# Kernel tuning notes

Measured on AMD Instinct MI355X. Metric: run time of the kernel, lower is better.

Reference implementation:

```python
import jax, jax.numpy as jnp
import numpy as np

DIM = 768
NUM_HEADS = 12
HEAD_DIM = DIM // NUM_HEADS
H, W = 16, 64
HK, WK = 7, 11
N = H * W
B = 8
SCALE = HEAD_DIM ** -0.5


def build_local_mask():
    # Vectorized version of the original nested loop: for each token (h,w),
    # positions inside the hk x wk window are visible (0), others -inf.
    h_idx = np.repeat(np.arange(H), W)  # [N]
    w_idx = np.tile(np.arange(W), H)    # [N]
    hh = np.arange(H + HK - 1)
    ww = np.arange(W + WK - 1)
    in_h = (hh[None, :] >= h_idx[:, None]) & (hh[None, :] < h_idx[:, None] + HK)  # [N, H+hk-1]
    in_w = (ww[None, :] >= w_idx[:, None]) & (ww[None, :] < w_idx[:, None] + WK)  # [N, W+wk-1]
    visible = in_h[:, :, None] & in_w[:, None, :]  # [N, H+hk-1, W+wk-1]
    mask_big = np.where(visible, 0.0, 1.0).astype(np.float32)
    mask_crop = mask_big[:, HK // 2:H + HK // 2, WK // 2:W + WK // 2].reshape(N, N)
    mask = np.where(mask_crop < 1.0, mask_crop, np.float32(-np.inf))  # [N, N]
    return jnp.asarray(mask)[None, None]  # [1, 1, N, N]


def setup_inputs() -> dict:
    key = jax.random.key(0)
    k1, k2, k3 = jax.random.split(key, 3)
    x = jax.random.normal(k1, (B, N, DIM), dtype=jnp.float32)
    w_qkv = jax.random.normal(k2, (3 * DIM, DIM), dtype=jnp.float32) * 0.02  # torch Linear weight [out,in]
    w_proj = jax.random.normal(k3, (DIM, DIM), dtype=jnp.float32) * 0.02
    b_proj = jnp.zeros((DIM,), dtype=jnp.float32)
    mask = build_local_mask()
    return {"x": x, "w_qkv": w_qkv, "w_proj": w_proj, "b_proj": b_proj, "mask": mask}


def reference(x, w_qkv, w_proj, b_proj, mask):
    Bx, Nx, C = x.shape
    qkv = jnp.einsum('bnc,oc->bno', x, w_qkv)  # [B, N, 3*dim]
    qkv = qkv.reshape(Bx, Nx, 3, NUM_HEADS, HEAD_DIM).transpose(2, 0, 3, 1, 4)  # [3,B,h,N,d]
    q, k, v = qkv[0] * SCALE, qkv[1], qkv[2]
    attn = jnp.einsum('bhnd,bhmd->bhnm', q, k) + mask  # [B,h,N,N] with local -inf mask
    attn = jax.nn.softmax(attn, axis=-1)
    out = jnp.einsum('bhnm,bhmd->bhnd', attn, v)  # [B,h,N,d]
    out = out.transpose(0, 2, 1, 3).reshape(Bx, Nx, C)
    out = jnp.einsum('bnc,oc->bno', out, w_proj) + b_proj
    return out
```

## Files before the change

### kernel.cpp

```cpp
#include <hip/hip_runtime.h>
#include <hip/hip_bf16.h>
#include <stdint.h>

typedef __bf16 bf16;
typedef __bf16 bf16x8 __attribute__((ext_vector_type(8)));
typedef __bf16 bf16x4 __attribute__((ext_vector_type(4)));
typedef float f32x4 __attribute__((ext_vector_type(4)));

#define KDIM 768
#define NHEAD 12
#define HDIM 64
#define NTOK 1024
#define BATCH 8

#define SWZ(row, b) ((b) ^ (((row) & 7) << 4))

__device__ __forceinline__ void gl_lds16(const bf16* g, bf16* l) {
    __builtin_amdgcn_global_load_lds((const __attribute__((address_space(1))) void*)g,
                                     (__attribute__((address_space(3))) void*)l, 16, 0, 0);
}

#define G_MFMA(a, b, c) __builtin_amdgcn_mfma_f32_16x16x32_bf16(a, b, c, 0, 0, 0)
#define VMW(N) asm volatile("s_waitcnt vmcnt(" #N ")" ::: "memory")

__global__ void k_cvt_all(const float* __restrict__ x, const float* __restrict__ wq,
                          const float* __restrict__ wp, bf16* __restrict__ xb,
                          bf16* __restrict__ wqb, bf16* __restrict__ wpb) {
    int b = blockIdx.x;
    const float* src;
    bf16* dst;
    int base;
    if (b < 6144)       { src = x;  dst = xb;  base = b; }
    else if (b < 7872)  { src = wq; dst = wqb; base = b - 6144; }
    else                { src = wp; dst = wpb; base = b - 7872; }
    int i = (base * 256 + threadIdx.x) * 4;
    float4 v = *(const float4*)(src + i);
    bf16x4 o;
    o[0] = (bf16)v.x; o[1] = (bf16)v.y; o[2] = (bf16)v.z; o[3] = (bf16)v.w;
    *(bf16x4*)(dst + i) = o;
}


#define QTILE(S, kA, kB, doA, doB, vmn) do {                                    \
    const char* A8 = (const char*)sA[S];                                        \
    const char* B8 = (const char*)sB[S];                                        \
    bf16x8 af[2], bfr[6];                                                       \
    af[0] = *(const bf16x8*)(A8 + (wr * 64 + 0 + lr) * 64 + kxoff);             \
    af[1] = *(const bf16x8*)(A8 + (wr * 64 + 16 + lr) * 64 + kxoff);            \
    _Pragma("unroll")                                                           \
    for (int n = 0; n < 6; ++n)                                                 \
        bfr[n] = *(const bf16x8*)(B8 + (wc * 96 + n * 16 + lr) * 64 + kxoff);   \
    if (doA) {                                                                  \
        const bf16* p_ = Ast + (size_t)(kA) * 32;                               \
        gl_lds16(p_,                    &sA[(S) ^ 1][t * 8]);                   \
        gl_lds16(p_ + (size_t)64 * KDIM, &sA[(S) ^ 1][t * 8 + 2048]);           \
    }                                                                           \
    __builtin_amdgcn_s_setprio(1);                                              \
    _Pragma("unroll")                                                           \
    for (int m = 0; m < 2; ++m)                                                 \
        _Pragma("unroll")                                                       \
        for (int n = 0; n < 6; ++n)                                             \
            acc[m][n] = G_MFMA(af[m], bfr[n], acc[m][n]);                       \
    __builtin_amdgcn_s_setprio(0);                                              \
    __builtin_amdgcn_s_barrier();                                               \
    af[0] = *(const bf16x8*)(A8 + (wr * 64 + 32 + lr) * 64 + kxoff);            \
    af[1] = *(const bf16x8*)(A8 + (wr * 64 + 48 + lr) * 64 + kxoff);            \
    if (doB) {                                                                  \
        const bf16* p_ = Wst + (size_t)(kB) * 32;                               \
        gl_lds16(p_,                     &sB[S][t * 8]);                        \
        gl_lds16(p_ + (size_t)64 * KDIM,  &sB[S][t * 8 + 2048]);                \
        gl_lds16(p_ + (size_t)128 * KDIM, &sB[S][t * 8 + 4096]);                \
    }                                                                           \
    __builtin_amdgcn_s_setprio(1);                                              \
    _Pragma("unroll")                                                           \
    for (int m = 0; m < 2; ++m)                                                 \
        _Pragma("unroll")                                                       \
        for (int n = 0; n < 6; ++n)                                             \
            acc[m + 2][n] = G_MFMA(af[m], bfr[n], acc[m + 2][n]);               \
    __builtin_amdgcn_s_setprio(0);                                              \
    if ((vmn) == 3) { VMW(3); } else if ((vmn) == 0) { VMW(0); }                \
    __builtin_amdgcn_s_barrier();                                               \
} while (0)

__global__ __launch_bounds__(256, 3) void k_gemm_qkv(
    const bf16* __restrict__ A, const bf16* __restrict__ W,
    bf16* __restrict__ qb, bf16* __restrict__ kb, bf16* __restrict__ vb)
{
    __shared__ __attribute__((aligned(16))) bf16 sA[2][4096];
    __shared__ __attribute__((aligned(16))) bf16 sB[2][6144];
    const int t = threadIdx.x;
    const int lane = t & 63;
    const int wv = t >> 6;
    const int wr = wv >> 1, wc = wv & 1;
    const int lr = lane & 15, lg = lane >> 4;
    const int kxoff = (lg << 4) ^ (((lr >> 1) & 3) << 4);
    const int srow = t >> 2;
    const int spos = ((t & 3) ^ ((t >> 3) & 3)) * 8;
    const int bm = blockIdx.x, bn = blockIdx.y;
    const bf16* Ab = A + (size_t)bm * 128 * KDIM;
    const bf16* Wb = W + (size_t)bn * 192 * KDIM;
    const bf16* Ast = Ab + (size_t)srow * KDIM + spos;
    const bf16* Wst = Wb + (size_t)srow * KDIM + spos;
    f32x4 acc[4][6] = {};

    gl_lds16(Ast,                     &sA[0][t * 8]);
    gl_lds16(Ast + (size_t)64 * KDIM, &sA[0][t * 8 + 2048]);
    gl_lds16(Wst,                      &sB[0][t * 8]);
    gl_lds16(Wst + (size_t)64 * KDIM,  &sB[0][t * 8 + 2048]);
    gl_lds16(Wst + (size_t)128 * KDIM, &sB[0][t * 8 + 4096]);
    gl_lds16(Wst + 32,                      &sB[1][t * 8]);
    gl_lds16(Wst + 32 + (size_t)64 * KDIM,  &sB[1][t * 8 + 2048]);
    gl_lds16(Wst + 32 + (size_t)128 * KDIM, &sB[1][t * 8 + 4096]);
    VMW(3);
    __builtin_amdgcn_s_barrier();

#pragma unroll 1
    for (int g = 0; g < 11; ++g) {
        QTILE(0, 2 * g + 1, 2 * g + 2, 1, 1, 3);
        QTILE(1, 2 * g + 2, 2 * g + 3, 1, 1, 3);
    }
    QTILE(0, 23, 0, 1, 0, 0);
    QTILE(1, 0, 0, 0, 0, -1);

    const float QSC = 0.18033688011112042f;
#pragma unroll
    for (int n = 0; n < 6; ++n) {
        int o = bn * 192 + wc * 96 + n * 16 + lr;
        int s = o / 768;
        int rem = o - s * 768;
        int head = rem >> 6;
        int d = o & 63;
        bf16* dst = (s == 0) ? qb : ((s == 1) ? kb : vb);
        float sc = (s == 0) ? QSC : 1.0f;
#pragma unroll
        for (int m = 0; m < 4; ++m) {
            int grow = bm * 128 + wr * 64 + m * 16 + lg * 4;
            int bidx = grow >> 10;
            int tok = grow & 1023;
            size_t base = (((size_t)bidx * NHEAD + head) * NTOK + tok) * HDIM + d;
#pragma unroll
            for (int r = 0; r < 4; ++r)
                dst[base + (size_t)r * HDIM] = (bf16)(acc[m][n][r] * sc);
        }
    }
}

#define P_STAGE(Ab, Wb, Abuf, Bbuf, k0) do {                                    \
    gl_lds16((Ab) + (size_t)sr0 * KDIM + (k0) + sc0, (Abuf) + wv * 512);        \
    gl_lds16((Ab) + (size_t)sr1 * KDIM + (k0) + sc1, (Abuf) + 2048 + wv * 512); \
    gl_lds16((Wb) + (size_t)sr0 * KDIM + (k0) + sc0, (Bbuf) + wv * 512);        \
    gl_lds16((Wb) + (size_t)sr1 * KDIM + (k0) + sc1, (Bbuf) + 2048 + wv * 512); \
} while (0)

__global__ __launch_bounds__(256) void k_gemm_proj(
    const bf16* __restrict__ A, const bf16* __restrict__ W,
    const float* __restrict__ bias, float* __restrict__ out)
{
    __shared__ bf16 As[2][4096];
    __shared__ bf16 Bs[2][4096];
    const int t = threadIdx.x;
    const int lane = t & 63;
    const int wv = t >> 6;
    const int wr = wv >> 1, wc = wv & 1;
    const int lr = lane & 15, lg = lane >> 4;
    const int q0 = wv * 64 + lane;
    const int R0 = q0 >> 3, wp0 = (q0 & 7) ^ (R0 & 7);
    const int sr0 = 2 * R0 + (wp0 >> 2), sc0 = (wp0 & 3) * 8;
    const int q1 = 256 + wv * 64 + lane;
    const int R1 = q1 >> 3, wp1 = (q1 & 7) ^ (R1 & 7);
    const int sr1 = 2 * R1 + (wp1 >> 2), sc1 = (wp1 & 3) * 8;
    const int rhalf = lr >> 1;
    const int xorp = (((lr & 1) * 64 + lg * 16) ^ (rhalf << 4));
    const int bm = blockIdx.x, bn = blockIdx.y;
    const bf16* Ab = A + (size_t)bm * 128 * KDIM;
    const bf16* Wb = W + (size_t)bn * 128 * KDIM;

    f32x4 acc[4][4] = {};
    P_STAGE(Ab, Wb, As[0], Bs[0], 0);
    P_STAGE(Ab, Wb, As[1], Bs[1], 32);
    VMW(4);
    __builtin_amdgcn_s_barrier();
#pragma unroll 1
    for (int tt = 0; tt < 24; ++tt) {
        int p = tt & 1;
        const char* Ab8 = (const char*)As[p];
        const char* Bb8 = (const char*)Bs[p];
        bf16x8 af[4], bfr[4];
#pragma unroll
        for (int m = 0; m < 4; ++m)
            af[m] = *(const bf16x8*)(Ab8 + (wr * 32 + m * 8 + rhalf) * 128 + xorp);
#pragma unroll
        for (int n = 0; n < 4; ++n)
            bfr[n] = *(const bf16x8*)(Bb8 + (wc * 32 + n * 8 + rhalf) * 128 + xorp);
        asm volatile("s_waitcnt lgkmcnt(0)" ::: "memory");
        __builtin_amdgcn_s_barrier();
        if (tt < 22) {
            P_STAGE(Ab, Wb, As[p], Bs[p], (tt + 2) * 32);
            __builtin_amdgcn_sched_barrier(0);
        }
#pragma unroll
        for (int m = 0; m < 4; ++m)
#pragma unroll
            for (int n = 0; n < 4; ++n)
                acc[m][n] = G_MFMA(af[m], bfr[n], acc[m][n]);
        if (tt < 22)       { VMW(4); }
        else if (tt == 22) { VMW(0); }
        __builtin_amdgcn_s_barrier();
    }

#pragma unroll
    for (int n = 0; n < 4; ++n) {
        int col = bn * 128 + wc * 64 + n * 16 + lr;
        float bv = bias[col];
#pragma unroll
        for (int m = 0; m < 4; ++m) {
            int grow = bm * 128 + wr * 64 + m * 16 + lg * 4;
#pragma unroll
            for (int r = 0; r < 4; ++r)
                out[(size_t)(grow + r) * KDIM + col] = acc[m][n][r] + bv;
        }
    }
}

__global__ __launch_bounds__(256) void k_attn(
    const bf16* __restrict__ qbuf, const bf16* __restrict__ kbuf,
    const bf16* __restrict__ vbuf, bf16* __restrict__ ob)
{
    const int x = blockIdx.x;
    const int sub = x >> 3;
    const int bh = (x & 7) * 12 + (sub >> 4);
    const int qblk = sub & 15;
    const int head = bh % NHEAD, bidx = bh / NHEAD;
    const bf16* Q  = qbuf + (size_t)bh * NTOK * HDIM;
    const bf16* Kp = kbuf + (size_t)bh * NTOK * HDIM;
    const bf16* Vp = vbuf + (size_t)bh * NTOK * HDIM;

    const int t = threadIdx.x, lane = t & 63, wv = t >> 6;
    const int lr = lane & 15, lg = lane >> 4, lkb = lg * 8;

    __shared__ bf16 Ks[2][64 * 64];
    __shared__ bf16 vT[2][64 * 64];
    __shared__ bf16 pls[4][16 * 64];

    {
        bf16x8 z = {};
        *(bf16x8*)&pls[wv][lane * 16] = z;
        *(bf16x8*)&pls[wv][lane * 16 + 8] = z;
    }

    bf16x8 qf[2];
#pragma unroll
    for (int ks = 0; ks < 2; ++ks)
        qf[ks] = *(const bf16x8*)(Q + (size_t)(qblk * 64 + wv * 16 + lr) * HDIM + ks * 32 + lkb);

    f32x4 acc[4] = {};
    float mrow[4] = {-1e30f, -1e30f, -1e30f, -1e30f};
    float lrow[4] = {0.f, 0.f, 0.f, 0.f};

    const int kh0 = (qblk - 3 < 0) ? 0 : qblk - 3;
    const int kh1 = (qblk + 3 > 15) ? 15 : qblk + 3;

    const int sj = t >> 2;
    const int sd = (t & 3) * 16;

    const bf16* ks0 = Kp + (size_t)(kh0 * 64 + sj) * HDIM + sd;
    const bf16* vs0 = Vp + (size_t)(kh0 * 64 + sj) * HDIM + sd;
    bf16x8 gk0 = *(const bf16x8*)ks0, gk1 = *(const bf16x8*)(ks0 + 8);
    bf16x8 gv0 = *(const bf16x8*)vs0, gv1 = *(const bf16x8*)(vs0 + 8);

    char* pb8 = (char*)pls[wv];
    const int wq0 = wv * 16 + lg * 4;
    int cur = 0;

    for (int kh = kh0; kh <= kh1; ++kh) {
        char* kb8 = (char*)Ks[cur];
        char* vb8 = (char*)vT[cur];
        {
            int kbo = sj * 128 + sd * 2;
            *(bf16x8*)(kb8 + SWZ(sj, kbo)) = gk0;
            *(bf16x8*)(kb8 + SWZ(sj, kbo + 16)) = gk1;
        }
#pragma unroll
        for (int ii = 0; ii < 8; ++ii) {
            int d = sd + ii;
            *(bf16*)(vb8 + SWZ(d, (d << 7) + (sj << 1))) = gv0[ii];
        }
#pragma unroll
        for (int ii = 0; ii < 8; ++ii) {
            int d = sd + 8 + ii;
            *(bf16*)(vb8 + SWZ(d, (d << 7) + (sj << 1))) = gv1[ii];
        }
        if (kh < kh1) {
            const bf16* kn = Kp + (size_t)((kh + 1) * 64 + sj) * HDIM + sd;
            const bf16* vn = Vp + (size_t)((kh + 1) * 64 + sj) * HDIM + sd;
            gk0 = *(const bf16x8*)kn; gk1 = *(const bf16x8*)(kn + 8);
            gv0 = *(const bf16x8*)vn; gv1 = *(const bf16x8*)(vn + 8);
        }
        asm volatile("s_waitcnt lgkmcnt(0)" ::: "memory");
        __builtin_amdgcn_s_barrier();

        f32x4 s[3];
#pragma unroll
        for (int jj = 0; jj < 3; ++jj) {
            int j = wv - 1 + jj;
            if (j >= 0 && j <= 3) {
                int key = j * 16 + lr;
                int kbase = key * 128;
                bf16x8 kf0 = *(const bf16x8*)(kb8 + SWZ(key, kbase + lg * 16));
                bf16x8 kf1 = *(const bf16x8*)(kb8 + SWZ(key, kbase + 64 + lg * 16));
                f32x4 sv = {};
                sv = __builtin_amdgcn_mfma_f32_16x16x32_bf16(qf[0], kf0, sv, 0, 0, 0);
                sv = __builtin_amdgcn_mfma_f32_16x16x32_bf16(qf[1], kf1, sv, 0, 0, 0);
#pragma unroll
                for (int r = 0; r < 4; ++r) {
                    int dw = wq0 + r - key;
                    sv[r] = (dw >= -5 && dw <= 5) ? sv[r] : -1e30f;
                }
                s[jj] = sv;
            } else {
                s[jj] = f32x4{-1e30f, -1e30f, -1e30f, -1e30f};
            }
        }

        float pm[4], scl[4];
#pragma unroll
        for (int r = 0; r < 4; ++r) pm[r] = fmaxf(fmaxf(s[0][r], s[1][r]), s[2][r]);
#pragma unroll
        for (int off = 1; off < 16; off <<= 1)
#pragma unroll
            for (int r = 0; r < 4; ++r) pm[r] = fmaxf(pm[r], __shfl_xor(pm[r], off));
#pragma unroll
        for (int r = 0; r < 4; ++r) {
            float mn = fmaxf(mrow[r], pm[r]);
            scl[r] = exp2f(mrow[r] - mn);
            mrow[r] = mn;
        }
#pragma unroll
        for (int dt = 0; dt < 4; ++dt)
#pragma unroll
            for (int r = 0; r < 4; ++r) acc[dt][r] *= scl[r];

        float psum[4] = {0.f, 0.f, 0.f, 0.f};
#pragma unroll
        for (int jj = 0; jj < 3; ++jj) {
            int j = wv - 1 + jj;
            if (j >= 0 && j <= 3) {
#pragma unroll
                for (int r = 0; r < 4; ++r) {
                    float p = exp2f(s[jj][r] - mrow[r]);
                    psum[r] += p;
                    int row = lg * 4 + r;
                    *(bf16*)(pb8 + SWZ(row, row * 128 + (j * 16 + lr) * 2)) = (bf16)p;
                }
            }
        }
#pragma unroll
        for (int r = 0; r < 4; ++r) lrow[r] = lrow[r] * scl[r] + psum[r];

        bf16x8 pf0 = *(const bf16x8*)(pb8 + SWZ(lr, lr * 128 + lg * 16));
        bf16x8 pf1 = *(const bf16x8*)(pb8 + SWZ(lr, lr * 128 + 64 + lg * 16));
#pragma unroll
        for (int dt = 0; dt < 4; ++dt) {
            int vrow = dt * 16 + lr;
            bf16x8 vf0 = *(const bf16x8*)(vb8 + SWZ(vrow, vrow * 128 + lg * 16));
            bf16x8 vf1 = *(const bf16x8*)(vb8 + SWZ(vrow, vrow * 128 + 64 + lg * 16));
            acc[dt] = __builtin_amdgcn_mfma_f32_16x16x32_bf16(pf0, vf0, acc[dt], 0, 0, 0);
            acc[dt] = __builtin_amdgcn_mfma_f32_16x16x32_bf16(pf1, vf1, acc[dt], 0, 0, 0);
        }
        cur ^= 1;
    }

#pragma unroll
    for (int off = 1; off < 16; off <<= 1)
#pragma unroll
        for (int r = 0; r < 4; ++r) lrow[r] += __shfl_xor(lrow[r], off);

#pragma unroll
    for (int r = 0; r < 4; ++r) {
        float inv = 1.0f / lrow[r];
        int tok = qblk * 64 + wv * 16 + lg * 4 + r;
        size_t rowbase = ((size_t)bidx * NTOK + tok) * KDIM + head * HDIM;
#pragma unroll
        for (int dt = 0; dt < 4; ++dt)
            ob[rowbase + dt * 16 + lr] = (bf16)(acc[dt][r] * inv);
    }
}

extern "C" void kernel_launch(void* const* d_in, const int* in_sizes, int n_in,
                              void* d_out, int out_size, void* d_ws, size_t ws_size,
                              hipStream_t stream) {
    const float* x      = (const float*)d_in[0];
    const float* w_qkv  = (const float*)d_in[1];
    const float* w_proj = (const float*)d_in[2];
    const float* b_proj = (const float*)d_in[3];
    float* out = (float*)d_out;

    char* ws = (char*)d_ws;
    bf16* xb  = (bf16*)(ws);
    bf16* wqb = (bf16*)(ws + 12582912);
    bf16* wpb = (bf16*)(ws + 16121856);
    bf16* qb  = (bf16*)(ws + 17301504);
    bf16* kb  = (bf16*)(ws + 29884416);
    bf16* vb  = (bf16*)(ws + 42467328);
    bf16* aob = (bf16*)(ws + 55050240);

    hipLaunchKernelGGL(k_cvt_all, dim3(8448), dim3(256), 0, stream, x, w_qkv, w_proj, xb, wqb, wpb);
    hipLaunchKernelGGL(k_gemm_qkv, dim3(64, 12), dim3(256), 0, stream, xb, wqb, qb, kb, vb);
    hipLaunchKernelGGL(k_attn,     dim3(1536), dim3(256), 0, stream, qb, kb, vb, aob);
    hipLaunchKernelGGL(k_gemm_proj, dim3(64, 6), dim3(256), 0, stream, aob, wpb, b_proj, out);
}
```

Baseline: 103.8 us.

## Fuse fp32 activation conversion into QKV GEMM and store interleaved QKV

The separate fp32-to-bf16 conversion of x is removed. The QKV GEMM now loads fp32 x into registers, converts it, and writes it to a triple-buffered LDS A tile, while the weights keep their async global-to-LDS path with a reworked wait schedule. The QKV output is written as a single token-major [B*N, 2304] buffer instead of head-split Q/K/V arrays, and attention reads from it with a 2304-element stride. This saves one full pass over x (read fp32, write and reread bf16), but it raises register pressure (occupancy hint drops from 3 to 2) and makes the attention K/V loads more strided.

```diff
diff --git a/kernel.cpp b/kernel.cpp
--- a/kernel.cpp
+++ b/kernel.cpp
@@ -12,6 +12,7 @@
 #define HDIM 64
 #define NTOK 1024
 #define BATCH 8
+#define QKVW 2304
 
 #define SWZ(row, b) ((b) ^ (((row) & 7) << 4))
 
@@ -23,16 +24,14 @@
 #define G_MFMA(a, b, c) __builtin_amdgcn_mfma_f32_16x16x32_bf16(a, b, c, 0, 0, 0)
 #define VMW(N) asm volatile("s_waitcnt vmcnt(" #N ")" ::: "memory")
 
-__global__ void k_cvt_all(const float* __restrict__ x, const float* __restrict__ wq,
-                          const float* __restrict__ wp, bf16* __restrict__ xb,
-                          bf16* __restrict__ wqb, bf16* __restrict__ wpb) {
+__global__ void k_cvt_w(const float* __restrict__ wq, const float* __restrict__ wp,
+                        bf16* __restrict__ wqb, bf16* __restrict__ wpb) {
     int b = blockIdx.x;
     const float* src;
     bf16* dst;
     int base;
-    if (b < 6144)       { src = x;  dst = xb;  base = b; }
-    else if (b < 7872)  { src = wq; dst = wqb; base = b - 6144; }
-    else                { src = wp; dst = wpb; base = b - 7872; }
+    if (b < 1728) { src = wq; dst = wqb; base = b; }
+    else          { src = wp; dst = wpb; base = b - 1728; }
     int i = (base * 256 + threadIdx.x) * 4;
     float4 v = *(const float4*)(src + i);
     bf16x4 o;
@@ -41,52 +40,74 @@
 }
 
 
-#define QTILE(S, kA, kB, doA, doB, vmn) do {                                    \
-    const char* A8 = (const char*)sA[S];                                        \
-    const char* B8 = (const char*)sB[S];                                        \
-    bf16x8 af[2], bfr[6];                                                       \
-    af[0] = *(const bf16x8*)(A8 + (wr * 64 + 0 + lr) * 64 + kxoff);             \
-    af[1] = *(const bf16x8*)(A8 + (wr * 64 + 16 + lr) * 64 + kxoff);            \
+#define AISS(R, kt) do {                                                        \
+    const float* p_ = Xst + (size_t)(kt) * 32;                                  \
+    R[0] = *(const float4*)(p_);                                                \
+    R[1] = *(const float4*)(p_ + 4);                                            \
+    R[2] = *(const float4*)(p_ + (size_t)64 * KDIM);                            \
+    R[3] = *(const float4*)(p_ + (size_t)64 * KDIM + 4);                        \
+} while (0)
+
+#define BISS(slot, kt) do {                                                     \
+    const bf16* p_ = Wst + (size_t)(kt) * 32;                                   \
+    gl_lds16(p_,                       &sB[slot][t * 8]);                       \
+    gl_lds16(p_ + (size_t)64 * KDIM,   &sB[slot][t * 8 + 2048]);                \
+    gl_lds16(p_ + (size_t)128 * KDIM,  &sB[slot][t * 8 + 4096]);                \
+} while (0)
+
+#define AWRT(R, slot) do {                                                      \
+    bf16x8 v0, v1;                                                              \
+    v0[0] = (bf16)R[0].x; v0[1] = (bf16)R[0].y; v0[2] = (bf16)R[0].z; v0[3] = (bf16)R[0].w; \
+    v0[4] = (bf16)R[1].x; v0[5] = (bf16)R[1].y; v0[6] = (bf16)R[1].z; v0[7] = (bf16)R[1].w; \
+    v1[0] = (bf16)R[2].x; v1[1] = (bf16)R[2].y; v1[2] = (bf16)R[2].z; v1[3] = (bf16)R[2].w; \
+    v1[4] = (bf16)R[3].x; v1[5] = (bf16)R[3].y; v1[6] = (bf16)R[3].z; v1[7] = (bf16)R[3].w; \
+    char* dp_ = (char*)&sA[0][0] + (slot) * 8192 + srow * 64 + swb;             \
+    *(bf16x8*)dp_ = v0;                                                         \
+    *(bf16x8*)(dp_ + 4096) = v1;                                                \
+} while (0)
+
+#define QTILE(ASL, BSL, RISS, RWRT, I_) do {                                    \
+    const int kt = g6 + (I_);                                                   \
+    const char* A8 = (const char*)sA[ASL];                                      \
+    const char* B8 = (const char*)sB[BSL];                                      \
+    bf16x8 af0 = *(const bf16x8*)(A8 + (wr * 64 +  0 + lr) * 64 + kxoff);       \
+    bf16x8 af1 = *(const bf16x8*)(A8 + (wr * 64 + 16 + lr) * 64 + kxoff);       \
+    bf16x8 af2 = *(const bf16x8*)(A8 + (wr * 64 + 32 + lr) * 64 + kxoff);       \
+    bf16x8 af3 = *(const bf16x8*)(A8 + (wr * 64 + 48 + lr) * 64 + kxoff);       \
+    bf16x8 bfr[6];                                                              \
     _Pragma("unroll")                                                           \
     for (int n = 0; n < 6; ++n)                                                 \
         bfr[n] = *(const bf16x8*)(B8 + (wc * 96 + n * 16 + lr) * 64 + kxoff);   \
-    if (doA) {                                                                  \
-        const bf16* p_ = Ast + (size_t)(kA) * 32;                               \
-        gl_lds16(p_,                    &sA[(S) ^ 1][t * 8]);                   \
-        gl_lds16(p_ + (size_t)64 * KDIM, &sA[(S) ^ 1][t * 8 + 2048]);           \
-    }                                                                           \
+    if (kt + 1 < 24) BISS((BSL) ^ 1, kt + 1);                                   \
+    if (kt + 2 < 24) AISS(RISS, kt + 2);                                        \
     __builtin_amdgcn_s_setprio(1);                                              \
     _Pragma("unroll")                                                           \
-    for (int m = 0; m < 2; ++m)                                                 \
-        _Pragma("unroll")                                                       \
-        for (int n = 0; n < 6; ++n)                                             \
-            acc[m][n] = G_MFMA(af[m], bfr[n], acc[m][n]);                       \
+    for (int n = 0; n < 6; ++n) {                                               \
+        acc[0][n] = G_MFMA(af0, bfr[n], acc[0][n]);                             \
+        acc[1][n] = G_MFMA(af1, bfr[n], acc[1][n]);                             \
+    }                                                                           \
     __builtin_amdgcn_s_setprio(0);                                              \
-    __builtin_amdgcn_s_barrier();                                               \
-    af[0] = *(const bf16x8*)(A8 + (wr * 64 + 32 + lr) * 64 + kxoff);            \
-    af[1] = *(const bf16x8*)(A8 + (wr * 64 + 48 + lr) * 64 + kxoff);            \
-    if (doB) {                                                                  \
-        const bf16* p_ = Wst + (size_t)(kB) * 32;                               \
-        gl_lds16(p_,                     &sB[S][t * 8]);                        \
-        gl_lds16(p_ + (size_t)64 * KDIM,  &sB[S][t * 8 + 2048]);                \
-        gl_lds16(p_ + (size_t)128 * KDIM, &sB[S][t * 8 + 4096]);                \
-    }                                                                           \
     __builtin_amdgcn_s_setprio(1);                                              \
     _Pragma("unroll")                                                           \
-    for (int m = 0; m < 2; ++m)                                                 \
-        _Pragma("unroll")                                                       \
-        for (int n = 0; n < 6; ++n)                                             \
-            acc[m + 2][n] = G_MFMA(af[m], bfr[n], acc[m + 2][n]);               \
+    for (int n = 0; n < 6; ++n) {                                               \
+        acc[2][n] = G_MFMA(af2, bfr[n], acc[2][n]);                             \
+        acc[3][n] = G_MFMA(af3, bfr[n], acc[3][n]);                             \
+    }                                                                           \
     __builtin_amdgcn_s_setprio(0);                                              \
-    if ((vmn) == 3) { VMW(3); } else if ((vmn) == 0) { VMW(0); }                \
-    __builtin_amdgcn_s_barrier();                                               \
+    if (kt < 22)       { VMW(4); }                                              \
+    else if (kt == 22) { VMW(0); }                                              \
+    if (kt < 23) {                                                              \
+        AWRT(RWRT, ((ASL) + 1) % 3);                                            \
+        asm volatile("s_waitcnt lgkmcnt(0)" ::: "memory");                      \
+        __builtin_amdgcn_s_barrier();                                           \
+    }                                                                           \
 } while (0)
 
-__global__ __launch_bounds__(256, 3) void k_gemm_qkv(
-    const bf16* __restrict__ A, const bf16* __restrict__ W,
-    bf16* __restrict__ qb, bf16* __restrict__ kb, bf16* __restrict__ vb)
+__global__ __launch_bounds__(256, 2) void k_gemm_qkv(
+    const float* __restrict__ X, const bf16* __restrict__ W,
+    bf16* __restrict__ qkvb)
 {
-    __shared__ __attribute__((aligned(16))) bf16 sA[2][4096];
+    __shared__ __attribute__((aligned(16))) bf16 sA[3][4096];
     __shared__ __attribute__((aligned(16))) bf16 sB[2][6144];
     const int t = threadIdx.x;
     const int lane = t & 63;
@@ -95,52 +116,45 @@
     const int lr = lane & 15, lg = lane >> 4;
     const int kxoff = (lg << 4) ^ (((lr >> 1) & 3) << 4);
     const int srow = t >> 2;
-    const int spos = ((t & 3) ^ ((t >> 3) & 3)) * 8;
+    const int swb = (((t & 3) ^ ((t >> 3) & 3))) << 4;
+    const int spos = (((t & 3) ^ ((t >> 3) & 3))) * 8;
     const int bm = blockIdx.x, bn = blockIdx.y;
-    const bf16* Ab = A + (size_t)bm * 128 * KDIM;
-    const bf16* Wb = W + (size_t)bn * 192 * KDIM;
-    const bf16* Ast = Ab + (size_t)srow * KDIM + spos;
-    const bf16* Wst = Wb + (size_t)srow * KDIM + spos;
+    const float* Xst = X + (size_t)(bm * 128 + srow) * KDIM + (t & 3) * 8;
+    const bf16* Wst  = W + (size_t)(bn * 192 + srow) * KDIM + spos;
     f32x4 acc[4][6] = {};
-
-    gl_lds16(Ast,                     &sA[0][t * 8]);
-    gl_lds16(Ast + (size_t)64 * KDIM, &sA[0][t * 8 + 2048]);
-    gl_lds16(Wst,                      &sB[0][t * 8]);
-    gl_lds16(Wst + (size_t)64 * KDIM,  &sB[0][t * 8 + 2048]);
-    gl_lds16(Wst + (size_t)128 * KDIM, &sB[0][t * 8 + 4096]);
-    gl_lds16(Wst + 32,                      &sB[1][t * 8]);
-    gl_lds16(Wst + 32 + (size_t)64 * KDIM,  &sB[1][t * 8 + 2048]);
-    gl_lds16(Wst + 32 + (size_t)128 * KDIM, &sB[1][t * 8 + 4096]);
+    float4 rE[4], rO[4];
+
+    AISS(rE, 0);
+    BISS(0, 0);
     VMW(3);
+    AWRT(rE, 0);
+    AISS(rE, 1);
+    VMW(4);
+    asm volatile("s_waitcnt lgkmcnt(0)" ::: "memory");
     __builtin_amdgcn_s_barrier();
 
 #pragma unroll 1
-    for (int g = 0; g < 11; ++g) {
-        QTILE(0, 2 * g + 1, 2 * g + 2, 1, 1, 3);
-        QTILE(1, 2 * g + 2, 2 * g + 3, 1, 1, 3);
-    }
-    QTILE(0, 23, 0, 1, 0, 0);
-    QTILE(1, 0, 0, 0, 0, -1);
+    for (int g = 0; g < 4; ++g) {
+        const int g6 = g * 6;
+        QTILE(0, 0, rO, rE, 0);
+        QTILE(1, 1, rE, rO, 1);
+        QTILE(2, 0, rO, rE, 2);
+        QTILE(0, 1, rE, rO, 3);
+        QTILE(1, 0, rO, rE, 4);
+        QTILE(2, 1, rE, rO, 5);
+    }
 
     const float QSC = 0.18033688011112042f;
 #pragma unroll
     for (int n = 0; n < 6; ++n) {
         int o = bn * 192 + wc * 96 + n * 16 + lr;
-        int s = o / 768;
-        int rem = o - s * 768;
-        int head = rem >> 6;
-        int d = o & 63;
-        bf16* dst = (s == 0) ? qb : ((s == 1) ? kb : vb);
-        float sc = (s == 0) ? QSC : 1.0f;
+        float sc = (o < 768) ? QSC : 1.0f;
 #pragma unroll
         for (int m = 0; m < 4; ++m) {
-            int grow = bm * 128 + wr * 64 + m * 16 + lg * 4;
-            int bidx = grow >> 10;
-            int tok = grow & 1023;
-            size_t base = (((size_t)bidx * NHEAD + head) * NTOK + tok) * HDIM + d;
+            int row = bm * 128 + wr * 64 + m * 16 + lg * 4;
 #pragma unroll
             for (int r = 0; r < 4; ++r)
-                dst[base + (size_t)r * HDIM] = (bf16)(acc[m][n][r] * sc);
+                qkvb[(size_t)(row + r) * QKVW + o] = (bf16)(acc[m][n][r] * sc);
         }
     }
 }
@@ -223,17 +237,14 @@
 }
 
 __global__ __launch_bounds__(256) void k_attn(
-    const bf16* __restrict__ qbuf, const bf16* __restrict__ kbuf,
-    const bf16* __restrict__ vbuf, bf16* __restrict__ ob)
+    const bf16* __restrict__ qkvb, bf16* __restrict__ ob)
 {
     const int x = blockIdx.x;
     const int sub = x >> 3;
     const int bh = (x & 7) * 12 + (sub >> 4);
     const int qblk = sub & 15;
     const int head = bh % NHEAD, bidx = bh / NHEAD;
-    const bf16* Q  = qbuf + (size_t)bh * NTOK * HDIM;
-    const bf16* Kp = kbuf + (size_t)bh * NTOK * HDIM;
-    const bf16* Vp = vbuf + (size_t)bh * NTOK * HDIM;
+    const bf16* BH = qkvb + (size_t)bidx * NTOK * QKVW + head * 64;
 
     const int t = threadIdx.x, lane = t & 63, wv = t >> 6;
     const int lr = lane & 15, lg = lane >> 4, lkb = lg * 8;
@@ -251,7 +262,7 @@
     bf16x8 qf[2];
 #pragma unroll
     for (int ks = 0; ks < 2; ++ks)
-        qf[ks] = *(const bf16x8*)(Q + (size_t)(qblk * 64 + wv * 16 + lr) * HDIM + ks * 32 + lkb);
+        qf[ks] = *(const bf16x8*)(BH + (size_t)(qblk * 64 + wv * 16 + lr) * QKVW + ks * 32 + lkb);
 
     f32x4 acc[4] = {};
     float mrow[4] = {-1e30f, -1e30f, -1e30f, -1e30f};
@@ -263,8 +274,8 @@
     const int sj = t >> 2;
     const int sd = (t & 3) * 16;
 
-    const bf16* ks0 = Kp + (size_t)(kh0 * 64 + sj) * HDIM + sd;
-    const bf16* vs0 = Vp + (size_t)(kh0 * 64 + sj) * HDIM + sd;
+    const bf16* ks0 = BH + 768 + (size_t)(kh0 * 64 + sj) * QKVW + sd;
+    const bf16* vs0 = BH + 1536 + (size_t)(kh0 * 64 + sj) * QKVW + sd;
     bf16x8 gk0 = *(const bf16x8*)ks0, gk1 = *(const bf16x8*)(ks0 + 8);
     bf16x8 gv0 = *(const bf16x8*)vs0, gv1 = *(const bf16x8*)(vs0 + 8);
 
@@ -291,8 +302,8 @@
             *(bf16*)(vb8 + SWZ(d, (d << 7) + (sj << 1))) = gv1[ii];
         }
         if (kh < kh1) {
-            const bf16* kn = Kp + (size_t)((kh + 1) * 64 + sj) * HDIM + sd;
-            const bf16* vn = Vp + (size_t)((kh + 1) * 64 + sj) * HDIM + sd;
+            const bf16* kn = BH + 768 + (size_t)((kh + 1) * 64 + sj) * QKVW + sd;
+            const bf16* vn = BH + 1536 + (size_t)((kh + 1) * 64 + sj) * QKVW + sd;
             gk0 = *(const bf16x8*)kn; gk1 = *(const bf16x8*)(kn + 8);
             gv0 = *(const bf16x8*)vn; gv1 = *(const bf16x8*)(vn + 8);
         }
@@ -396,16 +407,13 @@
     float* out = (float*)d_out;
 
     char* ws = (char*)d_ws;
-    bf16* xb  = (bf16*)(ws);
-    bf16* wqb = (bf16*)(ws + 12582912);
-    bf16* wpb = (bf16*)(ws + 16121856);
-    bf16* qb  = (bf16*)(ws + 17301504);
-    bf16* kb  = (bf16*)(ws + 29884416);
-    bf16* vb  = (bf16*)(ws + 42467328);
-    bf16* aob = (bf16*)(ws + 55050240);
-
-    hipLaunchKernelGGL(k_cvt_all, dim3(8448), dim3(256), 0, stream, x, w_qkv, w_proj, xb, wqb, wpb);
-    hipLaunchKernelGGL(k_gemm_qkv, dim3(64, 12), dim3(256), 0, stream, xb, wqb, qb, kb, vb);
-    hipLaunchKernelGGL(k_attn,     dim3(1536), dim3(256), 0, stream, qb, kb, vb, aob);
+    bf16* qkvb = (bf16*)(ws);
+    bf16* wqb  = (bf16*)(ws + 37748736);
+    bf16* wpb  = (bf16*)(ws + 41287680);
+    bf16* aob  = (bf16*)(ws + 42467328);
+
+    hipLaunchKernelGGL(k_cvt_w,    dim3(2304), dim3(256), 0, stream, w_qkv, w_proj, wqb, wpb);
+    hipLaunchKernelGGL(k_gemm_qkv, dim3(64, 12), dim3(256), 0, stream, x, wqb, qkvb);
+    hipLaunchKernelGGL(k_attn,     dim3(1536), dim3(256), 0, stream, qkvb, aob);
     hipLaunchKernelGGL(k_gemm_proj, dim3(64, 6), dim3(256), 0, stream, aob, wpb, b_proj, out);
 }
```

After: 113.7 us. 9.5% more time.
